# Kernel tuning notes

Hardware: AMD Instinct MI355X
Metric: run time of the kernel (lower is better)

The kernel has to match this reference:

```python
import jax, jax.numpy as jnp
import numpy as np

D_LATENT, D_HIDDEN, D_TIME, K = 128, 256, 16, 3
B, NX = 8, 4096
MSG_IN = 2 * D_LATENT + 1 + D_TIME + 2  # 275
UPD_IN = 2 * D_LATENT + D_TIME          # 272


def _gelu(v):
    return jax.nn.gelu(v, approximate=False)  # torch nn.GELU default (erf)


def _linear_params(key, din, dout):
    k1, k2 = jax.random.split(key)
    bound = 1.0 / np.sqrt(din)
    w = jax.random.uniform(k1, (din, dout), minval=-bound, maxval=bound, dtype=jnp.float32)
    b = jax.random.uniform(k2, (dout,), minval=-bound, maxval=bound, dtype=jnp.float32)
    return w, b


def setup_inputs() -> dict:
    key = jax.random.key(0)
    ks = jax.random.split(key, 16)
    inp = {
        'h': jax.random.normal(ks[0], (B, NX, D_LATENT), dtype=jnp.float32),
        'x': jax.random.uniform(ks[1], (B, NX), dtype=jnp.float32),
        'tau': jax.random.normal(ks[2], (B, D_TIME), dtype=jnp.float32),
        'u0': jax.random.normal(ks[3], (B, NX), dtype=jnp.float32),
    }
    inp['msg_w1'], inp['msg_b1'] = _linear_params(ks[4], MSG_IN, D_HIDDEN)
    inp['msg_w2'], inp['msg_b2'] = _linear_params(ks[5], D_HIDDEN, D_HIDDEN)
    inp['msg_w3'], inp['msg_b3'] = _linear_params(ks[6], D_HIDDEN, D_LATENT)
    inp['gate_w1'], inp['gate_b1'] = _linear_params(ks[7], MSG_IN, D_HIDDEN)
    inp['gate_w2'], inp['gate_b2'] = _linear_params(ks[8], D_HIDDEN, 1)
    inp['upd_w1'], inp['upd_b1'] = _linear_params(ks[9], UPD_IN, D_HIDDEN)
    inp['upd_w2'], inp['upd_b2'] = _linear_params(ks[10], D_HIDDEN, D_HIDDEN)
    inp['upd_w3'], inp['upd_b3'] = _linear_params(ks[11], D_HIDDEN, D_LATENT)
    inp['W_w'], inp['W_b'] = _linear_params(ks[12], D_LATENT, D_LATENT)
    return inp


def reference(h, x, tau, u0, msg_w1, msg_b1, msg_w2, msg_b2, msg_w3, msg_b3,
              gate_w1, gate_b1, gate_w2, gate_b2,
              upd_w1, upd_b1, upd_w2, upd_b2, upd_w3, upd_b3, W_w, W_b):
    Bq, nx, d = h.shape
    k = K
    S = 2 * k + 1
    # replicate padding along the spatial dim
    h_pad = jnp.pad(h, ((0, 0), (k, k), (0, 0)), mode='edge')
    x_pad = jnp.pad(x, ((0, 0), (k, k)), mode='edge')
    u0_pad = jnp.pad(u0, ((0, 0), (k, k)), mode='edge')
    # all stencil windows at once: idx[nx, S] gathers neighbor j for node i
    idx = jnp.arange(nx)[:, None] + jnp.arange(S)[None, :]
    h_j = h_pad[:, idx, :]                                  # [B, nx, S, d]
    rel = (x_pad[:, idx] - x[:, :, None])[..., None]        # [B, nx, S, 1]
    du0 = (u0[:, :, None] - u0_pad[:, idx])[..., None]      # [B, nx, S, 1]
    h_e = jnp.broadcast_to(h[:, :, None, :], (Bq, nx, S, d))
    tau_e = jnp.broadcast_to(tau[:, None, None, :], (Bq, nx, S, tau.shape[-1]))
    msg_in = jnp.concatenate([h_e, h_j, rel, tau_e, du0, jnp.abs(du0)], axis=-1)  # [B,nx,S,275]
    a = _gelu(msg_in @ msg_w1 + msg_b1)
    a = _gelu(a @ msg_w2 + msg_b2)
    msg = a @ msg_w3 + msg_b3                               # [B, nx, S, d]
    g = _gelu(msg_in @ gate_w1 + gate_b1)
    gate = jax.nn.sigmoid(g @ gate_w2 + gate_b2)            # [B, nx, S, 1]
    agg = jnp.sum(gate * msg, axis=2)                       # [B, nx, d]
    tau_n = jnp.broadcast_to(tau[:, None, :], (Bq, nx, tau.shape[-1]))
    upd_in = jnp.concatenate([h, agg, tau_n], axis=-1)      # [B, nx, 272]
    u = _gelu(upd_in @ upd_w1 + upd_b1)
    u = _gelu(u @ upd_w2 + upd_b2)
    h_nonlocal = u @ upd_w3 + upd_b3
    h_local = h @ W_w + W_b
    return _gelu(h_nonlocal + h_local)
```

## Files before the change

kernel.cpp:

```cpp
#include <hip/hip_runtime.h>
#include <hip/hip_bf16.h>
#include <math.h>

#define NXC 4096
#define NNODES 32768

typedef __attribute__((ext_vector_type(8))) short bf16x8;
typedef __attribute__((ext_vector_type(4))) short s16x4;
typedef __attribute__((ext_vector_type(16))) float f32x16;
typedef __attribute__((ext_vector_type(2))) float f32x2;

#define MFMA32(a,b,c) __builtin_amdgcn_mfma_f32_32x32x16_bf16((a),(b),(c),0,0,0)

#define GC4  3.359256e-5f
#define GC3 -0.000850511f
#define GC2  0.00941855f
#define GC1 -0.06622291f
#define GC0  0.3989423f

__device__ __forceinline__ float gelu_f(float x) {
    float xc = fminf(fmaxf(x, -3.0f), 3.0f);
    float s = xc * xc;
    float q = fmaf(s, GC4, GC3);
    q = fmaf(s, q, GC2);
    q = fmaf(s, q, GC1);
    q = fmaf(s, q, GC0);
    return x * fmaf(xc, q, 0.5f);
}
__device__ __forceinline__ f32x2 gelu2(f32x2 x) {
    const f32x2 lo = {-3.0f, -3.0f}, hi = {3.0f, 3.0f};
    const f32x2 c4 = {GC4, GC4}, c3 = {GC3, GC3}, c2 = {GC2, GC2};
    const f32x2 c1 = {GC1, GC1}, c0 = {GC0, GC0}, half = {0.5f, 0.5f};
    f32x2 xc = __builtin_elementwise_min(__builtin_elementwise_max(x, lo), hi);
    f32x2 s = xc * xc;
    f32x2 q = __builtin_elementwise_fma(s, c4, c3);
    q = __builtin_elementwise_fma(s, q, c2);
    q = __builtin_elementwise_fma(s, q, c1);
    q = __builtin_elementwise_fma(s, q, c0);
    return x * __builtin_elementwise_fma(xc, q, half);
}
__device__ __forceinline__ float sigmoid_f(float v) {
    float e = __builtin_amdgcn_exp2f(-1.4426950409f * v);
    return __builtin_amdgcn_rcpf(1.0f + e);
}
__device__ __forceinline__ short f2bs(float x) {
    __hip_bfloat16 b = __float2bfloat16(x);
    union { __hip_bfloat16 h; short s; } u; u.h = b; return u.s;
}
__device__ __forceinline__ f32x16 zero16() {
    f32x16 v;
    #pragma unroll
    for (int i = 0; i < 16; ++i) v[i] = 0.f;
    return v;
}
__device__ __forceinline__ float dpp_xor1(float x) {
    return __int_as_float(__builtin_amdgcn_update_dpp(0, __float_as_int(x), 0xB1, 0xF, 0xF, true));
}
__device__ __forceinline__ float dpp_xor2(float x) {
    return __int_as_float(__builtin_amdgcn_update_dpp(0, __float_as_int(x), 0x4E, 0xF, 0xF, true));
}

__global__ void wconv_kernel(const float* __restrict__ msg_w2, const float* __restrict__ msg_w3,
                             const float* __restrict__ msg_w1, const float* __restrict__ gate_w1,
                             const float* __restrict__ upd_w1, const float* __restrict__ upd_w2,
                             const float* __restrict__ upd_w3, const float* __restrict__ W_w,
                             const float* __restrict__ tau,
                             const float* __restrict__ msg_b1, const float* __restrict__ gate_b1,
                             const float* __restrict__ upd_b1,
                             __hip_bfloat16* __restrict__ w2t, __hip_bfloat16* __restrict__ w3t,
                             __hip_bfloat16* __restrict__ wall_t, __hip_bfloat16* __restrict__ w1ut,
                             __hip_bfloat16* __restrict__ w2ut, __hip_bfloat16* __restrict__ w3ut,
                             __hip_bfloat16* __restrict__ wwt,
                             float* __restrict__ TM, float* __restrict__ TG, float* __restrict__ TU)
{
    if (blockIdx.x >= 1600) {
        const int b = blockIdx.x - 1600;
        const int t = threadIdx.x;
        float tv[16];
        #pragma unroll
        for (int k = 0; k < 16; ++k) tv[k] = tau[b*16 + k];
        float am = msg_b1[t], ag = gate_b1[t], au = upd_b1[t];
        #pragma unroll
        for (int k = 0; k < 16; ++k) {
            am = fmaf(tv[k], msg_w1 [(257+k)*256 + t], am);
            ag = fmaf(tv[k], gate_w1[(257+k)*256 + t], ag);
            au = fmaf(tv[k], upd_w1 [(256+k)*256 + t], au);
        }
        TM[b*256+t] = am; TG[b*256+t] = ag; TU[b*256+t] = au;
        return;
    }
    int i = blockIdx.x * 256 + threadIdx.x;
    if (i < 65536) { int c=i>>8, k=i&255; w2t[i] = __float2bfloat16(msg_w2[k*256+c]); return; }
    i -= 65536;
    if (i < 32768) { int c=i>>8, k=i&255; w3t[i] = __float2bfloat16(msg_w3[k*128+c]); return; }
    i -= 32768;
    if (i < 131072) {
        int c = i>>7, k = i&127; float v;
        if      (c <  256) v = msg_w1 [k*256 + c];
        else if (c <  512) v = msg_w1 [(128+k)*256 + (c-256)];
        else if (c <  768) v = gate_w1[k*256 + (c-512)];
        else               v = gate_w1[(128+k)*256 + (c-768)];
        wall_t[i] = __float2bfloat16(v); return;
    }
    i -= 131072;
    if (i < 65536) { int c=i>>8, k=i&255; w1ut[i] = __float2bfloat16(upd_w1[k*256+c]); return; }
    i -= 65536;
    if (i < 65536) { int c=i>>8, k=i&255; w2ut[i] = __float2bfloat16(upd_w2[k*256+c]); return; }
    i -= 65536;
    if (i < 32768) { int c=i>>8, k=i&255; w3ut[i] = __float2bfloat16(upd_w3[k*128+c]); return; }
    i -= 32768;
    { int c=i>>7, k=i&127; wwt[i] = __float2bfloat16(W_w[k*128+c]); }
}

#define PSTR 136

__global__ __launch_bounds__(256, 3)
void precompute_kernel(const float* __restrict__ h, const __hip_bfloat16* __restrict__ wall_t,
                       __hip_bfloat16* __restrict__ PAm, __hip_bfloat16* __restrict__ PBm,
                       __hip_bfloat16* __restrict__ PAg, __hip_bfloat16* __restrict__ PBg)
{
    __shared__ __align__(16) __hip_bfloat16 hs[64*PSTR];
    __shared__ __align__(16) __hip_bfloat16 ob[64*256];
    const int t = threadIdx.x;
    const int lane = t & 63, wv = t >> 6;
    const int cl = lane & 31, g = lane >> 5;
    const int base = blockIdx.x * 64;

    #pragma unroll
    for (int i = 0; i < 8; ++i) {
        int f = (i*256 + t)*4;
        float4 hv = *(const float4*)&h[(size_t)base*128 + f];
        int row = f >> 7, col = f & 127;
        s16x4 pk; pk[0]=f2bs(hv.x); pk[1]=f2bs(hv.y); pk[2]=f2bs(hv.z); pk[3]=f2bs(hv.w);
        *(s16x4*)&hs[row*PSTR + col] = pk;
    }
    __syncthreads();

    __hip_bfloat16* bufs[4] = {PAm, PBm, PAg, PBg};
    const int c0 = wv*64 + cl, c1 = c0 + 32;
    const __hip_bfloat16* a0  = hs + (size_t)(cl)*PSTR + g*8;
    const __hip_bfloat16* a1p = hs + (size_t)(32+cl)*PSTR + g*8;

    for (int tile = 0; tile < 4; ++tile) {
        f32x16 a00 = zero16(), a01 = zero16(), a10 = zero16(), a11 = zero16();
        {
            const __hip_bfloat16* b0 = wall_t + ((size_t)tile*256 + c0)*128 + g*8;
            const __hip_bfloat16* b1 = wall_t + ((size_t)tile*256 + c1)*128 + g*8;
            #pragma unroll
            for (int kt = 0; kt < 8; ++kt) {
                bf16x8 bf0 = *(const bf16x8*)(b0 + kt*16);
                bf16x8 bf1 = *(const bf16x8*)(b1 + kt*16);
                bf16x8 af0 = *(const bf16x8*)(a0 + kt*16);
                bf16x8 af1 = *(const bf16x8*)(a1p + kt*16);
                a00 = MFMA32(af0, bf0, a00);
                a01 = MFMA32(af0, bf1, a01);
                a10 = MFMA32(af1, bf0, a10);
                a11 = MFMA32(af1, bf1, a11);
            }
        }
        #pragma unroll
        for (int r = 0; r < 16; ++r) {
            int row = (r&3) + 8*(r>>2) + 4*g;
            ob[row*256 + c0]      = __float2bfloat16(a00[r]);
            ob[row*256 + c1]      = __float2bfloat16(a01[r]);
            ob[(32+row)*256 + c0] = __float2bfloat16(a10[r]);
            ob[(32+row)*256 + c1] = __float2bfloat16(a11[r]);
        }
        __syncthreads();
        __hip_bfloat16* dst = bufs[tile];
        #pragma unroll
        for (int i = 0; i < 8; ++i) {
            int idx = i*256 + t;
            int row = idx >> 5, ch = idx & 31;
            *(float4*)&dst[(size_t)(base+row)*256 + ch*8] =
                *(const float4*)&ob[row*256 + ch*8];
        }
        __syncthreads();
    }
}

#define ENPB 8
#define EEPB 56
#define ARS  264
#define MRS  132

__global__ __launch_bounds__(256, 4)
void edge_kernel(const float* __restrict__ x, const float* __restrict__ u0,
                 const float* __restrict__ msg_w1, const float* __restrict__ gate_w1,
                 const __hip_bfloat16* __restrict__ w2t, const float* __restrict__ msg_b2,
                 const __hip_bfloat16* __restrict__ w3t, const float* __restrict__ msg_b3,
                 const float* __restrict__ gate_w2, const float* __restrict__ gate_b2,
                 const __hip_bfloat16* __restrict__ PAm, const __hip_bfloat16* __restrict__ PBm,
                 const __hip_bfloat16* __restrict__ PAg, const __hip_bfloat16* __restrict__ PBg,
                 const float* __restrict__ TM, const float* __restrict__ TG,
                 __hip_bfloat16* __restrict__ AGG)
{
    __shared__ __align__(16) __hip_bfloat16 act[64*ARS];
    __shared__ __align__(16) float s_rel[EEPB], s_du[EEPB], s_ad[EEPB];
    __shared__ float s_gp[4][EEPB];
    __shared__ int   s_slotj[14];
    __shared__ float s_gate[EEPB];

    const int t    = threadIdx.x;
    const int lane = t & 63;
    const int wv   = t >> 6;
    const int base = blockIdx.x * ENPB;
    const int b    = base >> 12;
    const int ii0  = base & (NXC-1);

    if (t < 14) {
        int jj = ii0 - 3 + t;
        jj = jj < 0 ? 0 : (jj > NXC-1 ? NXC-1 : jj);
        s_slotj[t] = b*NXC + jj;
    }
    if (t < EEPB) {
        int nd = t / 7, s = t - nd*7;
        int i  = base + nd;
        int jj = ii0 + nd + s - 3;
        jj = jj < 0 ? 0 : (jj > NXC-1 ? NXC-1 : jj);
        int j = b*NXC + jj;
        float rel = x[j] - x[i];
        float du  = u0[i] - u0[j];
        s_rel[t] = rel; s_du[t] = du; s_ad[t] = fabsf(du);
    }
    __syncthreads();

    {
        float wr  = msg_w1 [256*256+t], wd  = msg_w1 [273*256+t], wa  = msg_w1 [274*256+t];
        float gwr = gate_w1[256*256+t], gwd = gate_w1[273*256+t], gwa = gate_w1[274*256+t];
        float tm = TM[b*256+t], tg = TG[b*256+t];
        float g2 = gate_w2[t];
        const f32x2 wr2  = {wr, wr},  wd2  = {wd, wd},  wa2  = {wa, wa};
        const f32x2 gwr2 = {gwr,gwr}, gwd2 = {gwd,gwd}, gwa2 = {gwa,gwa};
        const f32x2 g22  = {g2, g2};
        float bm[14], bg[14], pam[8], pag[8], sacc[14];
        #pragma unroll
        for (int q = 0; q < 14; ++q) {
            size_t o = (size_t)s_slotj[q]*256 + t;
            bm[q] = __bfloat162float(PBm[o]) + tm;
            bg[q] = __bfloat162float(PBg[o]) + tg;
        }
        #pragma unroll
        for (int nd = 0; nd < 8; ++nd) {
            size_t o = (size_t)(base+nd)*256 + t;
            pam[nd] = __bfloat162float(PAm[o]);
            pag[nd] = __bfloat162float(PAg[o]);
        }
        const bool p1 = (lane & 1), p2 = ((lane & 2) != 0);
        #pragma unroll
        for (int mq = 0; mq < 14; ++mq) {
            float gq[4];
            #pragma unroll
            for (int pp = 0; pp < 2; ++pp) {
                const int e0 = mq*4 + pp*2, e1 = e0 + 1;
                const int nd0 = e0/7, q0 = nd0 + (e0 - nd0*7);
                const int nd1 = e1/7, q1 = nd1 + (e1 - nd1*7);
                f32x2 rel = *(const f32x2*)&s_rel[e0];
                f32x2 du  = *(const f32x2*)&s_du[e0];
                f32x2 ad  = *(const f32x2*)&s_ad[e0];
                f32x2 pm; pm[0] = pam[nd0] + bm[q0]; pm[1] = pam[nd1] + bm[q1];
                pm = __builtin_elementwise_fma(rel, wr2, pm);
                pm = __builtin_elementwise_fma(du,  wd2, pm);
                pm = __builtin_elementwise_fma(ad,  wa2, pm);
                f32x2 gm = gelu2(pm);
                act[e0*ARS + t] = __float2bfloat16(gm[0]);
                act[e1*ARS + t] = __float2bfloat16(gm[1]);
                f32x2 pg; pg[0] = pag[nd0] + bg[q0]; pg[1] = pag[nd1] + bg[q1];
                pg = __builtin_elementwise_fma(rel, gwr2, pg);
                pg = __builtin_elementwise_fma(du,  gwd2, pg);
                pg = __builtin_elementwise_fma(ad,  gwa2, pg);
                f32x2 gg = gelu2(pg) * g22;
                gq[pp*2] = gg[0]; gq[pp*2+1] = gg[1];
            }
            float xx = p1 ? gq[1] : gq[0], yy = p1 ? gq[0] : gq[1];
            xx += dpp_xor1(yy);
            float zz = p1 ? gq[3] : gq[2], ww = p1 ? gq[2] : gq[3];
            zz += dpp_xor1(ww);
            float uu = p2 ? zz : xx, vv = p2 ? xx : zz;
            uu += dpp_xor2(vv);
            sacc[mq] = uu;
        }
        #pragma unroll
        for (int m = 0; m < 14; ++m) {
            float v = sacc[m];
            v += __shfl_xor(v, 4);
            v += __shfl_xor(v, 8);
            v += __shfl_xor(v, 16);
            v += __shfl_xor(v, 32);
            if (lane < 4) s_gp[wv][m*4 + lane] = v;
        }
    }
    __syncthreads();
    if (t < EEPB)
        s_gate[t] = sigmoid_f(s_gp[0][t] + s_gp[1][t] + s_gp[2][t] + s_gp[3][t] + gate_b2[0]);

    const int cl = lane & 31;
    const int g  = lane >> 5;
    f32x16 acc00 = zero16(), acc01 = zero16(), acc10 = zero16(), acc11 = zero16();
    {
        const __hip_bfloat16* w2a = w2t + (size_t)((wv*2+0)*32 + cl)*256 + g*8;
        const __hip_bfloat16* w2b = w2t + (size_t)((wv*2+1)*32 + cl)*256 + g*8;
        const __hip_bfloat16* a1a = act + (size_t)(cl)*ARS + g*8;
        const __hip_bfloat16* a1b = act + (size_t)(32+cl)*ARS + g*8;
        #pragma unroll
        for (int kt = 0; kt < 16; ++kt) {
            bf16x8 bfa = *(const bf16x8*)(w2a + kt*16);
            bf16x8 bfb = *(const bf16x8*)(w2b + kt*16);
            bf16x8 afa = *(const bf16x8*)(a1a + kt*16);
            bf16x8 afb = *(const bf16x8*)(a1b + kt*16);
            acc00 = MFMA32(afa, bfa, acc00);
            acc01 = MFMA32(afa, bfb, acc01);
            acc10 = MFMA32(afb, bfa, acc10);
            acc11 = MFMA32(afb, bfb, acc11);
        }
    }
    __syncthreads();
    {
        const int c0 = (wv*2+0)*32 + cl;
        const int c1 = (wv*2+1)*32 + cl;
        float b20 = msg_b2[c0], b21 = msg_b2[c1];
        #pragma unroll
        for (int r = 0; r < 16; r += 2) {
            int row0 = (r&3) + 8*(r>>2) + 4*g;
            f32x2 v0 = {acc00[r] + b20, acc00[r+1] + b20};
            f32x2 g0 = gelu2(v0);
            act[row0*ARS + c0]     = __float2bfloat16(g0[0]);
            act[(row0+1)*ARS + c0] = __float2bfloat16(g0[1]);
            f32x2 v1 = {acc01[r] + b21, acc01[r+1] + b21};
            f32x2 g1 = gelu2(v1);
            act[row0*ARS + c1]     = __float2bfloat16(g1[0]);
            act[(row0+1)*ARS + c1] = __float2bfloat16(g1[1]);
            if (r < 12) {
                int row1 = 32 + row0;
                f32x2 v2 = {acc10[r] + b20, acc10[r+1] + b20};
                f32x2 g2v = gelu2(v2);
                act[row1*ARS + c0]     = __float2bfloat16(g2v[0]);
                act[(row1+1)*ARS + c0] = __float2bfloat16(g2v[1]);
                f32x2 v3 = {acc11[r] + b21, acc11[r+1] + b21};
                f32x2 g3 = gelu2(v3);
                act[row1*ARS + c1]     = __float2bfloat16(g3[0]);
                act[(row1+1)*ARS + c1] = __float2bfloat16(g3[1]);
            }
        }
    }
    __syncthreads();

    f32x16 m0 = zero16(), m1 = zero16();
    {
        const __hip_bfloat16* w3p = w3t + (size_t)(wv*32 + cl)*256 + g*8;
        const __hip_bfloat16* a2a = act + (size_t)(cl)*ARS + g*8;
        const __hip_bfloat16* a2b = act + (size_t)(32+cl)*ARS + g*8;
        #pragma unroll
        for (int kt = 0; kt < 16; ++kt) {
            bf16x8 bfr = *(const bf16x8*)(w3p + kt*16);
            m0 = MFMA32(*(const bf16x8*)(a2a + kt*16), bfr, m0);
            m1 = MFMA32(*(const bf16x8*)(a2b + kt*16), bfr, m1);
        }
    }
    __syncthreads();
    float* msgbuf = (float*)act;
    {
        const int c = wv*32 + cl;
        float b3v = msg_b3[c];
        #pragma unroll
        for (int r = 0; r < 16; r += 2) {
            int row0 = (r&3) + 8*(r>>2) + 4*g;
            f32x2 mm = {m0[r] + b3v, m0[r+1] + b3v};
            f32x2 gt = {s_gate[row0], s_gate[row0+1]};
            mm *= gt;
            msgbuf[row0*MRS + c]     = mm[0];
            msgbuf[(row0+1)*MRS + c] = mm[1];
            int row1 = 32 + row0;
            if (row1 + 1 < EEPB) {
                f32x2 nn = {m1[r] + b3v, m1[r+1] + b3v};
                f32x2 ht = {s_gate[row1], s_gate[row1+1]};
                nn *= ht;
                msgbuf[row1*MRS + c]     = nn[0];
                msgbuf[(row1+1)*MRS + c] = nn[1];
            }
        }
    }
    __syncthreads();

    {
        const int c2  = (t & 63) * 2;
        const int grp = t >> 6;
        #pragma unroll
        for (int p = 0; p < 2; ++p) {
            int nd = grp + p*4;
            f32x2 s = {0.f, 0.f};
            #pragma unroll
            for (int q2 = 0; q2 < 7; ++q2)
                s += *(const f32x2*)&msgbuf[(nd*7+q2)*MRS + c2];
            ushort2 u;
            u.x = (unsigned short)f2bs(s[0]);
            u.y = (unsigned short)f2bs(s[1]);
            *(ushort2*)&AGG[(size_t)(base+nd)*128 + c2] = u;
        }
    }
}

#define UM 32

__global__ __launch_bounds__(256, 4)
void update_kernel(const __hip_bfloat16* __restrict__ w1ut, const __hip_bfloat16* __restrict__ w2ut,
                   const __hip_bfloat16* __restrict__ w3ut, const __hip_bfloat16* __restrict__ wwt,
                   const float* __restrict__ upd_b2, const float* __restrict__ upd_b3,
                   const float* __restrict__ W_b,
                   const float* __restrict__ h, const __hip_bfloat16* __restrict__ AGG,
                   const float* __restrict__ TU,
                   float* __restrict__ out)
{
    __shared__ __align__(16) __hip_bfloat16 ub[UM*ARS];
    const int t = threadIdx.x;
    const int lane = t & 63, wv = t >> 6;
    const int cl = lane & 31, g = lane >> 5;
    const int base = blockIdx.x * UM;
    const int b = base >> 12;

    #pragma unroll
    for (int i = 0; i < 4; ++i) {
        int f = (i*256 + t)*4;
        int row = f >> 7, col = f & 127;
        float4 hv = *(const float4*)&h[(size_t)base*128 + f];
        s16x4 pk; pk[0]=f2bs(hv.x); pk[1]=f2bs(hv.y); pk[2]=f2bs(hv.z); pk[3]=f2bs(hv.w);
        *(s16x4*)&ub[row*ARS + col] = pk;
    }
    #pragma unroll
    for (int i = 0; i < 2; ++i) {
        int idx = i*256 + t;
        int row = idx >> 4, ch = idx & 15;
        *(float4*)&ub[row*ARS + 128 + ch*8] =
            *(const float4*)&AGG[(size_t)(base+row)*128 + ch*8];
    }
    __syncthreads();

    f32x16 u0a = zero16(), u1a = zero16(), hl = zero16();
    {
        const __hip_bfloat16* a0 = ub + (size_t)(cl)*ARS + g*8;
        const __hip_bfloat16* b0 = w1ut + (size_t)(wv*64 + cl)*256 + g*8;
        const __hip_bfloat16* b1 = w1ut + (size_t)(wv*64 + 32 + cl)*256 + g*8;
        const __hip_bfloat16* bw = wwt + (size_t)(wv*32 + cl)*128 + g*8;
        #pragma unroll
        for (int kt = 0; kt < 16; ++kt) {
            bf16x8 af = *(const bf16x8*)(a0 + kt*16);
            u0a = MFMA32(af, *(const bf16x8*)(b0 + kt*16), u0a);
            u1a = MFMA32(af, *(const bf16x8*)(b1 + kt*16), u1a);
            if (kt < 8)
                hl = MFMA32(af, *(const bf16x8*)(bw + kt*16), hl);
        }
    }
    __syncthreads();
    {
        const int c0 = wv*64 + cl, c1 = c0 + 32;
        float tu0 = TU[b*256 + c0], tu1 = TU[b*256 + c1];
        #pragma unroll
        for (int r = 0; r < 16; r += 2) {
            int row = (r&3) + 8*(r>>2) + 4*g;
            f32x2 v0 = {u0a[r] + tu0, u0a[r+1] + tu0};
            f32x2 g0 = gelu2(v0);
            ub[row*ARS + c0]     = __float2bfloat16(g0[0]);
            ub[(row+1)*ARS + c0] = __float2bfloat16(g0[1]);
            f32x2 v1 = {u1a[r] + tu1, u1a[r+1] + tu1};
            f32x2 g1 = gelu2(v1);
            ub[row*ARS + c1]     = __float2bfloat16(g1[0]);
            ub[(row+1)*ARS + c1] = __float2bfloat16(g1[1]);
        }
    }
    __syncthreads();

    f32x16 v0a = zero16(), v1a = zero16();
    {
        const __hip_bfloat16* a0 = ub + (size_t)(cl)*ARS + g*8;
        const __hip_bfloat16* b0 = w2ut + (size_t)(wv*64 + cl)*256 + g*8;
        const __hip_bfloat16* b1 = w2ut + (size_t)(wv*64 + 32 + cl)*256 + g*8;
        #pragma unroll
        for (int kt = 0; kt < 16; ++kt) {
            bf16x8 af = *(const bf16x8*)(a0 + kt*16);
            v0a = MFMA32(af, *(const bf16x8*)(b0 + kt*16), v0a);
            v1a = MFMA32(af, *(const bf16x8*)(b1 + kt*16), v1a);
        }
    }
    __syncthreads();
    {
        const int c0 = wv*64 + cl, c1 = c0 + 32;
        float b20 = upd_b2[c0], b21 = upd_b2[c1];
        #pragma unroll
        for (int r = 0; r < 16; r += 2) {
            int row = (r&3) + 8*(r>>2) + 4*g;
            f32x2 v0 = {v0a[r] + b20, v0a[r+1] + b20};
            f32x2 g0 = gelu2(v0);
            ub[row*ARS + c0]     = __float2bfloat16(g0[0]);
            ub[(row+1)*ARS + c0] = __float2bfloat16(g0[1]);
            f32x2 v1 = {v1a[r] + b21, v1a[r+1] + b21};
            f32x2 g1 = gelu2(v1);
            ub[row*ARS + c1]     = __float2bfloat16(g1[0]);
            ub[(row+1)*ARS + c1] = __float2bfloat16(g1[1]);
        }
    }
    __syncthreads();

    f32x16 w0a = zero16();
    {
        const __hip_bfloat16* wp = w3ut + (size_t)(wv*32 + cl)*256 + g*8;
        const __hip_bfloat16* a0 = ub + (size_t)(cl)*ARS + g*8;
        #pragma unroll
        for (int kt = 0; kt < 16; ++kt)
            w0a = MFMA32(*(const bf16x8*)(a0 + kt*16), *(const bf16x8*)(wp + kt*16), w0a);
    }
    {
        const int c = wv*32 + cl;
        float b3v = upd_b3[c] + W_b[c];
        #pragma unroll
        for (int r = 0; r < 16; r += 2) {
            int row = (r&3) + 8*(r>>2) + 4*g;
            f32x2 vv = {w0a[r] + b3v + hl[r], w0a[r+1] + b3v + hl[r+1]};
            f32x2 gg = gelu2(vv);
            size_t o0 = (size_t)(base+row)*128 + c;
            size_t o1 = (size_t)(base+row+1)*128 + c;
            out[o0] = gg[0];
            out[o1] = gg[1];
        }
    }
}

extern "C" void kernel_launch(void* const* d_in, const int* in_sizes, int n_in,
                              void* d_out, int out_size, void* d_ws, size_t ws_size,
                              hipStream_t stream)
{
    const float* h      = (const float*)d_in[0];
    const float* x      = (const float*)d_in[1];
    const float* tau    = (const float*)d_in[2];
    const float* u0     = (const float*)d_in[3];
    const float* msg_w1 = (const float*)d_in[4];
    const float* msg_b1 = (const float*)d_in[5];
    const float* msg_w2 = (const float*)d_in[6];
    const float* msg_b2 = (const float*)d_in[7];
    const float* msg_w3 = (const float*)d_in[8];
    const float* msg_b3 = (const float*)d_in[9];
    const float* gate_w1= (const float*)d_in[10];
    const float* gate_b1= (const float*)d_in[11];
    const float* gate_w2= (const float*)d_in[12];
    const float* gate_b2= (const float*)d_in[13];
    const float* upd_w1 = (const float*)d_in[14];
    const float* upd_b1 = (const float*)d_in[15];
    const float* upd_w2 = (const float*)d_in[16];
    const float* upd_b2 = (const float*)d_in[17];
    const float* upd_w3 = (const float*)d_in[18];
    const float* upd_b3 = (const float*)d_in[19];
    const float* W_w    = (const float*)d_in[20];
    const float* W_b    = (const float*)d_in[21];
    float* out = (float*)d_out;

    char* ws = (char*)d_ws;
    size_t off = 0;
    auto alloc = [&](size_t bytes) -> void* {
        void* p = ws + off;
        off += (bytes + 255) & ~(size_t)255;
        return p;
    };
    __hip_bfloat16* PAm = (__hip_bfloat16*)alloc((size_t)NNODES*256*2);
    __hip_bfloat16* PBm = (__hip_bfloat16*)alloc((size_t)NNODES*256*2);
    __hip_bfloat16* PAg = (__hip_bfloat16*)alloc((size_t)NNODES*256*2);
    __hip_bfloat16* PBg = (__hip_bfloat16*)alloc((size_t)NNODES*256*2);
    __hip_bfloat16* AGG = (__hip_bfloat16*)alloc((size_t)NNODES*128*2);
    float* TM  = (float*)alloc(8*256*4);
    float* TG  = (float*)alloc(8*256*4);
    float* TU  = (float*)alloc(8*256*4);
    __hip_bfloat16* w2t   = (__hip_bfloat16*)alloc((size_t)256*256*2);
    __hip_bfloat16* w3t   = (__hip_bfloat16*)alloc((size_t)128*256*2);
    __hip_bfloat16* wall_t= (__hip_bfloat16*)alloc((size_t)1024*128*2);
    __hip_bfloat16* w1ut  = (__hip_bfloat16*)alloc((size_t)256*256*2);
    __hip_bfloat16* w2ut  = (__hip_bfloat16*)alloc((size_t)256*256*2);
    __hip_bfloat16* w3ut  = (__hip_bfloat16*)alloc((size_t)128*256*2);
    __hip_bfloat16* wwt   = (__hip_bfloat16*)alloc((size_t)128*128*2);
    (void)ws_size; (void)in_sizes; (void)n_in; (void)out_size;

    wconv_kernel<<<1608, 256, 0, stream>>>(msg_w2, msg_w3, msg_w1, gate_w1,
                                           upd_w1, upd_w2, upd_w3, W_w,
                                           tau, msg_b1, gate_b1, upd_b1,
                                           w2t, w3t, wall_t, w1ut, w2ut, w3ut, wwt,
                                           TM, TG, TU);
    precompute_kernel<<<NNODES/64, 256, 0, stream>>>(h, wall_t,
                                                     PAm, PBm, PAg, PBg);
    edge_kernel<<<NNODES/ENPB, 256, 0, stream>>>(x, u0, msg_w1, gate_w1,
                                                 w2t, msg_b2, w3t, msg_b3,
                                                 gate_w2, gate_b2,
                                                 PAm, PBm, PAg, PBg, TM, TG, AGG);
    update_kernel<<<NNODES/UM, 256, 0, stream>>>(w1ut, w2ut, w3ut, wwt,
                                                 upd_b2, upd_b3, W_b,
                                                 h, AGG, TU, out);
}
```

Before: 201.3 us.

## Double block size to 512 threads and repartition MFMA tiles across eight waves

Launches the precompute, edge and update kernels with 512 threads instead of 256. Each wave now owns fewer output tiles (one 32-column slice instead of two), so accumulator register pressure drops and more waves share the same LDS tile. The update kernel doubles its rows per block to 64. The edge kernel splits its 56 edges across two thread halves for the layer-1 elementwise work. The intent is better latency hiding and occupancy, at the cost of more per-wave weight-fragment loads and fewer distinct blocks.

```diff
diff --git a/kernel.cpp b/kernel.cpp
--- a/kernel.cpp
+++ b/kernel.cpp
@@ -114,7 +114,7 @@
 
 #define PSTR 136
 
-__global__ __launch_bounds__(256, 3)
+__global__ __launch_bounds__(512, 6)
 void precompute_kernel(const float* __restrict__ h, const __hip_bfloat16* __restrict__ wall_t,
                        __hip_bfloat16* __restrict__ PAm, __hip_bfloat16* __restrict__ PBm,
                        __hip_bfloat16* __restrict__ PAg, __hip_bfloat16* __restrict__ PBg)
@@ -127,8 +127,8 @@
     const int base = blockIdx.x * 64;
 
     #pragma unroll
-    for (int i = 0; i < 8; ++i) {
-        int f = (i*256 + t)*4;
+    for (int i = 0; i < 4; ++i) {
+        int f = (i*512 + t)*4;
         float4 hv = *(const float4*)&h[(size_t)base*128 + f];
         int row = f >> 7, col = f & 127;
         s16x4 pk; pk[0]=f2bs(hv.x); pk[1]=f2bs(hv.y); pk[2]=f2bs(hv.z); pk[3]=f2bs(hv.w);
@@ -137,40 +137,32 @@
     __syncthreads();
 
     __hip_bfloat16* bufs[4] = {PAm, PBm, PAg, PBg};
-    const int c0 = wv*64 + cl, c1 = c0 + 32;
+    const int c0 = wv*32 + cl;
     const __hip_bfloat16* a0  = hs + (size_t)(cl)*PSTR + g*8;
     const __hip_bfloat16* a1p = hs + (size_t)(32+cl)*PSTR + g*8;
 
     for (int tile = 0; tile < 4; ++tile) {
-        f32x16 a00 = zero16(), a01 = zero16(), a10 = zero16(), a11 = zero16();
+        f32x16 acc0 = zero16(), acc1 = zero16();
         {
             const __hip_bfloat16* b0 = wall_t + ((size_t)tile*256 + c0)*128 + g*8;
-            const __hip_bfloat16* b1 = wall_t + ((size_t)tile*256 + c1)*128 + g*8;
             #pragma unroll
             for (int kt = 0; kt < 8; ++kt) {
-                bf16x8 bf0 = *(const bf16x8*)(b0 + kt*16);
-                bf16x8 bf1 = *(const bf16x8*)(b1 + kt*16);
-                bf16x8 af0 = *(const bf16x8*)(a0 + kt*16);
-                bf16x8 af1 = *(const bf16x8*)(a1p + kt*16);
-                a00 = MFMA32(af0, bf0, a00);
-                a01 = MFMA32(af0, bf1, a01);
-                a10 = MFMA32(af1, bf0, a10);
-                a11 = MFMA32(af1, bf1, a11);
+                bf16x8 bf = *(const bf16x8*)(b0 + kt*16);
+                acc0 = MFMA32(*(const bf16x8*)(a0  + kt*16), bf, acc0);
+                acc1 = MFMA32(*(const bf16x8*)(a1p + kt*16), bf, acc1);
             }
         }
         #pragma unroll
         for (int r = 0; r < 16; ++r) {
             int row = (r&3) + 8*(r>>2) + 4*g;
-            ob[row*256 + c0]      = __float2bfloat16(a00[r]);
-            ob[row*256 + c1]      = __float2bfloat16(a01[r]);
-            ob[(32+row)*256 + c0] = __float2bfloat16(a10[r]);
-            ob[(32+row)*256 + c1] = __float2bfloat16(a11[r]);
+            ob[row*256 + c0]      = __float2bfloat16(acc0[r]);
+            ob[(32+row)*256 + c0] = __float2bfloat16(acc1[r]);
         }
         __syncthreads();
         __hip_bfloat16* dst = bufs[tile];
         #pragma unroll
-        for (int i = 0; i < 8; ++i) {
-            int idx = i*256 + t;
+        for (int i = 0; i < 4; ++i) {
+            int idx = i*512 + t;
             int row = idx >> 5, ch = idx & 31;
             *(float4*)&dst[(size_t)(base+row)*256 + ch*8] =
                 *(const float4*)&ob[row*256 + ch*8];
@@ -184,7 +176,7 @@
 #define ARS  264
 #define MRS  132
 
-__global__ __launch_bounds__(256, 4)
+__global__ __launch_bounds__(512, 8)
 void edge_kernel(const float* __restrict__ x, const float* __restrict__ u0,
                  const float* __restrict__ msg_w1, const float* __restrict__ gate_w1,
                  const __hip_bfloat16* __restrict__ w2t, const float* __restrict__ msg_b2,
@@ -197,7 +189,7 @@
 {
     __shared__ __align__(16) __hip_bfloat16 act[64*ARS];
     __shared__ __align__(16) float s_rel[EEPB], s_du[EEPB], s_ad[EEPB];
-    __shared__ float s_gp[4][EEPB];
+    __shared__ float s_gp[8][28];
     __shared__ int   s_slotj[14];
     __shared__ float s_gate[EEPB];
 
@@ -226,46 +218,49 @@
     __syncthreads();
 
     {
-        float wr  = msg_w1 [256*256+t], wd  = msg_w1 [273*256+t], wa  = msg_w1 [274*256+t];
-        float gwr = gate_w1[256*256+t], gwd = gate_w1[273*256+t], gwa = gate_w1[274*256+t];
-        float tm = TM[b*256+t], tg = TG[b*256+t];
-        float g2 = gate_w2[t];
+        const int col  = t & 255;
+        const int half = t >> 8;
+        float wr  = msg_w1 [256*256+col], wd  = msg_w1 [273*256+col], wa  = msg_w1 [274*256+col];
+        float gwr = gate_w1[256*256+col], gwd = gate_w1[273*256+col], gwa = gate_w1[274*256+col];
+        float tm = TM[b*256+col], tg = TG[b*256+col];
+        float g2 = gate_w2[col];
         const f32x2 wr2  = {wr, wr},  wd2  = {wd, wd},  wa2  = {wa, wa};
         const f32x2 gwr2 = {gwr,gwr}, gwd2 = {gwd,gwd}, gwa2 = {gwa,gwa};
         const f32x2 g22  = {g2, g2};
-        float bm[14], bg[14], pam[8], pag[8], sacc[14];
-        #pragma unroll
-        for (int q = 0; q < 14; ++q) {
-            size_t o = (size_t)s_slotj[q]*256 + t;
+        float bm[10], bg[10], pam[4], pag[4], sacc[7];
+        #pragma unroll
+        for (int q = 0; q < 10; ++q) {
+            size_t o = (size_t)s_slotj[half*4 + q]*256 + col;
             bm[q] = __bfloat162float(PBm[o]) + tm;
             bg[q] = __bfloat162float(PBg[o]) + tg;
         }
         #pragma unroll
-        for (int nd = 0; nd < 8; ++nd) {
-            size_t o = (size_t)(base+nd)*256 + t;
-            pam[nd] = __bfloat162float(PAm[o]);
-            pag[nd] = __bfloat162float(PAg[o]);
+        for (int ndl = 0; ndl < 4; ++ndl) {
+            size_t o = (size_t)(base + half*4 + ndl)*256 + col;
+            pam[ndl] = __bfloat162float(PAm[o]);
+            pag[ndl] = __bfloat162float(PAg[o]);
         }
         const bool p1 = (lane & 1), p2 = ((lane & 2) != 0);
         #pragma unroll
-        for (int mq = 0; mq < 14; ++mq) {
+        for (int mq = 0; mq < 7; ++mq) {
             float gq[4];
             #pragma unroll
             for (int pp = 0; pp < 2; ++pp) {
-                const int e0 = mq*4 + pp*2, e1 = e0 + 1;
-                const int nd0 = e0/7, q0 = nd0 + (e0 - nd0*7);
-                const int nd1 = e1/7, q1 = nd1 + (e1 - nd1*7);
+                const int el0 = mq*4 + pp*2, el1 = el0 + 1;
+                const int e0 = half*28 + el0, e1 = e0 + 1;
+                const int ndl0 = el0/7, q0 = ndl0 + (el0 - ndl0*7);
+                const int ndl1 = el1/7, q1 = ndl1 + (el1 - ndl1*7);
                 f32x2 rel = *(const f32x2*)&s_rel[e0];
                 f32x2 du  = *(const f32x2*)&s_du[e0];
                 f32x2 ad  = *(const f32x2*)&s_ad[e0];
-                f32x2 pm; pm[0] = pam[nd0] + bm[q0]; pm[1] = pam[nd1] + bm[q1];
+                f32x2 pm; pm[0] = pam[ndl0] + bm[q0]; pm[1] = pam[ndl1] + bm[q1];
                 pm = __builtin_elementwise_fma(rel, wr2, pm);
                 pm = __builtin_elementwise_fma(du,  wd2, pm);
                 pm = __builtin_elementwise_fma(ad,  wa2, pm);
                 f32x2 gm = gelu2(pm);
-                act[e0*ARS + t] = __float2bfloat16(gm[0]);
-                act[e1*ARS + t] = __float2bfloat16(gm[1]);
-                f32x2 pg; pg[0] = pag[nd0] + bg[q0]; pg[1] = pag[nd1] + bg[q1];
+                act[e0*ARS + col] = __float2bfloat16(gm[0]);
+                act[e1*ARS + col] = __float2bfloat16(gm[1]);
+                f32x2 pg; pg[0] = pag[ndl0] + bg[q0]; pg[1] = pag[ndl1] + bg[q1];
                 pg = __builtin_elementwise_fma(rel, gwr2, pg);
                 pg = __builtin_elementwise_fma(du,  gwd2, pg);
                 pg = __builtin_elementwise_fma(ad,  gwa2, pg);
@@ -281,7 +276,7 @@
             sacc[mq] = uu;
         }
         #pragma unroll
-        for (int m = 0; m < 14; ++m) {
+        for (int m = 0; m < 7; ++m) {
             float v = sacc[m];
             v += __shfl_xor(v, 4);
             v += __shfl_xor(v, 8);
@@ -291,118 +286,94 @@
         }
     }
     __syncthreads();
-    if (t < EEPB)
-        s_gate[t] = sigmoid_f(s_gp[0][t] + s_gp[1][t] + s_gp[2][t] + s_gp[3][t] + gate_b2[0]);
+    if (t < EEPB) {
+        int hf = t / 28, el = t - hf*28;
+        float v = s_gp[hf*4+0][el] + s_gp[hf*4+1][el] + s_gp[hf*4+2][el] + s_gp[hf*4+3][el]
+                + gate_b2[0];
+        s_gate[t] = sigmoid_f(v);
+    }
 
     const int cl = lane & 31;
     const int g  = lane >> 5;
-    f32x16 acc00 = zero16(), acc01 = zero16(), acc10 = zero16(), acc11 = zero16();
-    {
-        const __hip_bfloat16* w2a = w2t + (size_t)((wv*2+0)*32 + cl)*256 + g*8;
-        const __hip_bfloat16* w2b = w2t + (size_t)((wv*2+1)*32 + cl)*256 + g*8;
+    f32x16 acc0 = zero16(), acc1 = zero16();
+    {
+        const __hip_bfloat16* w2p = w2t + (size_t)(wv*32 + cl)*256 + g*8;
         const __hip_bfloat16* a1a = act + (size_t)(cl)*ARS + g*8;
         const __hip_bfloat16* a1b = act + (size_t)(32+cl)*ARS + g*8;
         #pragma unroll
         for (int kt = 0; kt < 16; ++kt) {
-            bf16x8 bfa = *(const bf16x8*)(w2a + kt*16);
-            bf16x8 bfb = *(const bf16x8*)(w2b + kt*16);
-            bf16x8 afa = *(const bf16x8*)(a1a + kt*16);
-            bf16x8 afb = *(const bf16x8*)(a1b + kt*16);
-            acc00 = MFMA32(afa, bfa, acc00);
-            acc01 = MFMA32(afa, bfb, acc01);
-            acc10 = MFMA32(afb, bfa, acc10);
-            acc11 = MFMA32(afb, bfb, acc11);
-        }
-    }
-    __syncthreads();
-    {
-        const int c0 = (wv*2+0)*32 + cl;
-        const int c1 = (wv*2+1)*32 + cl;
-        float b20 = msg_b2[c0], b21 = msg_b2[c1];
+            bf16x8 bf = *(const bf16x8*)(w2p + kt*16);
+            acc0 = MFMA32(*(const bf16x8*)(a1a + kt*16), bf, acc0);
+            acc1 = MFMA32(*(const bf16x8*)(a1b + kt*16), bf, acc1);
+        }
+    }
+    __syncthreads();
+    {
+        const int c0 = wv*32 + cl;
+        float b20 = msg_b2[c0];
         #pragma unroll
         for (int r = 0; r < 16; r += 2) {
             int row0 = (r&3) + 8*(r>>2) + 4*g;
-            f32x2 v0 = {acc00[r] + b20, acc00[r+1] + b20};
+            f32x2 v0 = {acc0[r] + b20, acc0[r+1] + b20};
             f32x2 g0 = gelu2(v0);
             act[row0*ARS + c0]     = __float2bfloat16(g0[0]);
             act[(row0+1)*ARS + c0] = __float2bfloat16(g0[1]);
-            f32x2 v1 = {acc01[r] + b21, acc01[r+1] + b21};
-            f32x2 g1 = gelu2(v1);
-            act[row0*ARS + c1]     = __float2bfloat16(g1[0]);
-            act[(row0+1)*ARS + c1] = __float2bfloat16(g1[1]);
             if (r < 12) {
                 int row1 = 32 + row0;
-                f32x2 v2 = {acc10[r] + b20, acc10[r+1] + b20};
-                f32x2 g2v = gelu2(v2);
-                act[row1*ARS + c0]     = __float2bfloat16(g2v[0]);
-                act[(row1+1)*ARS + c0] = __float2bfloat16(g2v[1]);
-                f32x2 v3 = {acc11[r] + b21, acc11[r+1] + b21};
-                f32x2 g3 = gelu2(v3);
-                act[row1*ARS + c1]     = __float2bfloat16(g3[0]);
-                act[(row1+1)*ARS + c1] = __float2bfloat16(g3[1]);
+                f32x2 v1 = {acc1[r] + b20, acc1[r+1] + b20};
+                f32x2 g1 = gelu2(v1);
+                act[row1*ARS + c0]     = __float2bfloat16(g1[0]);
+                act[(row1+1)*ARS + c0] = __float2bfloat16(g1[1]);
             }
         }
     }
     __syncthreads();
 
-    f32x16 m0 = zero16(), m1 = zero16();
-    {
-        const __hip_bfloat16* w3p = w3t + (size_t)(wv*32 + cl)*256 + g*8;
-        const __hip_bfloat16* a2a = act + (size_t)(cl)*ARS + g*8;
-        const __hip_bfloat16* a2b = act + (size_t)(32+cl)*ARS + g*8;
-        #pragma unroll
-        for (int kt = 0; kt < 16; ++kt) {
-            bf16x8 bfr = *(const bf16x8*)(w3p + kt*16);
-            m0 = MFMA32(*(const bf16x8*)(a2a + kt*16), bfr, m0);
-            m1 = MFMA32(*(const bf16x8*)(a2b + kt*16), bfr, m1);
-        }
+    f32x16 m0 = zero16();
+    const int mt = wv >> 2, nt = wv & 3;
+    {
+        const __hip_bfloat16* w3p = w3t + (size_t)(nt*32 + cl)*256 + g*8;
+        const __hip_bfloat16* a2p = act + (size_t)(mt*32 + cl)*ARS + g*8;
+        #pragma unroll
+        for (int kt = 0; kt < 16; ++kt)
+            m0 = MFMA32(*(const bf16x8*)(a2p + kt*16), *(const bf16x8*)(w3p + kt*16), m0);
     }
     __syncthreads();
     float* msgbuf = (float*)act;
     {
-        const int c = wv*32 + cl;
+        const int c = nt*32 + cl;
         float b3v = msg_b3[c];
         #pragma unroll
         for (int r = 0; r < 16; r += 2) {
-            int row0 = (r&3) + 8*(r>>2) + 4*g;
-            f32x2 mm = {m0[r] + b3v, m0[r+1] + b3v};
-            f32x2 gt = {s_gate[row0], s_gate[row0+1]};
-            mm *= gt;
-            msgbuf[row0*MRS + c]     = mm[0];
-            msgbuf[(row0+1)*MRS + c] = mm[1];
-            int row1 = 32 + row0;
-            if (row1 + 1 < EEPB) {
-                f32x2 nn = {m1[r] + b3v, m1[r+1] + b3v};
-                f32x2 ht = {s_gate[row1], s_gate[row1+1]};
-                nn *= ht;
-                msgbuf[row1*MRS + c]     = nn[0];
-                msgbuf[(row1+1)*MRS + c] = nn[1];
+            int row0 = mt*32 + (r&3) + 8*(r>>2) + 4*g;
+            if (row0 + 1 < EEPB) {
+                f32x2 mm = {m0[r] + b3v, m0[r+1] + b3v};
+                f32x2 gt = {s_gate[row0], s_gate[row0+1]};
+                mm *= gt;
+                msgbuf[row0*MRS + c]     = mm[0];
+                msgbuf[(row0+1)*MRS + c] = mm[1];
             }
         }
     }
     __syncthreads();
 
     {
-        const int c2  = (t & 63) * 2;
-        const int grp = t >> 6;
-        #pragma unroll
-        for (int p = 0; p < 2; ++p) {
-            int nd = grp + p*4;
-            f32x2 s = {0.f, 0.f};
-            #pragma unroll
-            for (int q2 = 0; q2 < 7; ++q2)
-                s += *(const f32x2*)&msgbuf[(nd*7+q2)*MRS + c2];
-            ushort2 u;
-            u.x = (unsigned short)f2bs(s[0]);
-            u.y = (unsigned short)f2bs(s[1]);
-            *(ushort2*)&AGG[(size_t)(base+nd)*128 + c2] = u;
-        }
-    }
-}
-
-#define UM 32
-
-__global__ __launch_bounds__(256, 4)
+        const int c2 = (t & 63) * 2;
+        const int nd = wv;
+        f32x2 s = {0.f, 0.f};
+        #pragma unroll
+        for (int q2 = 0; q2 < 7; ++q2)
+            s += *(const f32x2*)&msgbuf[(nd*7+q2)*MRS + c2];
+        ushort2 u;
+        u.x = (unsigned short)f2bs(s[0]);
+        u.y = (unsigned short)f2bs(s[1]);
+        *(ushort2*)&AGG[(size_t)(base+nd)*128 + c2] = u;
+    }
+}
+
+#define UM 64
+
+__global__ __launch_bounds__(512, 6)
 void update_kernel(const __hip_bfloat16* __restrict__ w1ut, const __hip_bfloat16* __restrict__ w2ut,
                    const __hip_bfloat16* __restrict__ w3ut, const __hip_bfloat16* __restrict__ wwt,
                    const float* __restrict__ upd_b2, const float* __restrict__ upd_b3,
@@ -417,10 +388,11 @@
     const int cl = lane & 31, g = lane >> 5;
     const int base = blockIdx.x * UM;
     const int b = base >> 12;
+    const int mt = wv >> 2, nt = wv & 3;
 
     #pragma unroll
     for (int i = 0; i < 4; ++i) {
-        int f = (i*256 + t)*4;
+        int f = (i*512 + t)*4;
         int row = f >> 7, col = f & 127;
         float4 hv = *(const float4*)&h[(size_t)base*128 + f];
         s16x4 pk; pk[0]=f2bs(hv.x); pk[1]=f2bs(hv.y); pk[2]=f2bs(hv.z); pk[3]=f2bs(hv.w);
@@ -428,7 +400,7 @@
     }
     #pragma unroll
     for (int i = 0; i < 2; ++i) {
-        int idx = i*256 + t;
+        int idx = i*512 + t;
         int row = idx >> 4, ch = idx & 15;
         *(float4*)&ub[row*ARS + 128 + ch*8] =
             *(const float4*)&AGG[(size_t)(base+row)*128 + ch*8];
@@ -437,23 +409,24 @@
 
     f32x16 u0a = zero16(), u1a = zero16(), hl = zero16();
     {
-        const __hip_bfloat16* a0 = ub + (size_t)(cl)*ARS + g*8;
-        const __hip_bfloat16* b0 = w1ut + (size_t)(wv*64 + cl)*256 + g*8;
-        const __hip_bfloat16* b1 = w1ut + (size_t)(wv*64 + 32 + cl)*256 + g*8;
-        const __hip_bfloat16* bw = wwt + (size_t)(wv*32 + cl)*128 + g*8;
+        const __hip_bfloat16* a0  = ub + (size_t)(cl)*ARS + g*8;
+        const __hip_bfloat16* a1p = ub + (size_t)(32+cl)*ARS + g*8;
+        const __hip_bfloat16* ahl = ub + (size_t)(mt*32+cl)*ARS + g*8;
+        const __hip_bfloat16* b0 = w1ut + (size_t)(wv*32 + cl)*256 + g*8;
+        const __hip_bfloat16* bw = wwt + (size_t)(nt*32 + cl)*128 + g*8;
         #pragma unroll
         for (int kt = 0; kt < 16; ++kt) {
-            bf16x8 af = *(const bf16x8*)(a0 + kt*16);
-            u0a = MFMA32(af, *(const bf16x8*)(b0 + kt*16), u0a);
-            u1a = MFMA32(af, *(const bf16x8*)(b1 + kt*16), u1a);
+            bf16x8 bf = *(const bf16x8*)(b0 + kt*16);
+            u0a = MFMA32(*(const bf16x8*)(a0  + kt*16), bf, u0a);
+            u1a = MFMA32(*(const bf16x8*)(a1p + kt*16), bf, u1a);
             if (kt < 8)
-                hl = MFMA32(af, *(const bf16x8*)(bw + kt*16), hl);
-        }
-    }
-    __syncthreads();
-    {
-        const int c0 = wv*64 + cl, c1 = c0 + 32;
-        float tu0 = TU[b*256 + c0], tu1 = TU[b*256 + c1];
+                hl = MFMA32(*(const bf16x8*)(ahl + kt*16), *(const bf16x8*)(bw + kt*16), hl);
+        }
+    }
+    __syncthreads();
+    {
+        const int c0 = wv*32 + cl;
+        float tu0 = TU[b*256 + c0];
         #pragma unroll
         for (int r = 0; r < 16; r += 2) {
             int row = (r&3) + 8*(r>>2) + 4*g;
@@ -461,30 +434,30 @@
             f32x2 g0 = gelu2(v0);
             ub[row*ARS + c0]     = __float2bfloat16(g0[0]);
             ub[(row+1)*ARS + c0] = __float2bfloat16(g0[1]);
-            f32x2 v1 = {u1a[r] + tu1, u1a[r+1] + tu1};
+            f32x2 v1 = {u1a[r] + tu0, u1a[r+1] + tu0};
             f32x2 g1 = gelu2(v1);
-            ub[row*ARS + c1]     = __float2bfloat16(g1[0]);
-            ub[(row+1)*ARS + c1] = __float2bfloat16(g1[1]);
+            ub[(32+row)*ARS + c0]   = __float2bfloat16(g1[0]);
+            ub[(32+row+1)*ARS + c0] = __float2bfloat16(g1[1]);
         }
     }
     __syncthreads();
 
     f32x16 v0a = zero16(), v1a = zero16();
     {
-        const __hip_bfloat16* a0 = ub + (size_t)(cl)*ARS + g*8;
-        const __hip_bfloat16* b0 = w2ut + (size_t)(wv*64 + cl)*256 + g*8;
-        const __hip_bfloat16* b1 = w2ut + (size_t)(wv*64 + 32 + cl)*256 + g*8;
+        const __hip_bfloat16* a0  = ub + (size_t)(cl)*ARS + g*8;
+        const __hip_bfloat16* a1p = ub + (size_t)(32+cl)*ARS + g*8;
+        const __hip_bfloat16* b0 = w2ut + (size_t)(wv*32 + cl)*256 + g*8;
         #pragma unroll
         for (int kt = 0; kt < 16; ++kt) {
-            bf16x8 af = *(const bf16x8*)(a0 + kt*16);
-            v0a = MFMA32(af, *(const bf16x8*)(b0 + kt*16), v0a);
-            v1a = MFMA32(af, *(const bf16x8*)(b1 + kt*16), v1a);
-        }
-    }
-    __syncthreads();
-    {
-        const int c0 = wv*64 + cl, c1 = c0 + 32;
-        float b20 = upd_b2[c0], b21 = upd_b2[c1];
+            bf16x8 bf = *(const bf16x8*)(b0 + kt*16);
+            v0a = MFMA32(*(const bf16x8*)(a0  + kt*16), bf, v0a);
+            v1a = MFMA32(*(const bf16x8*)(a1p + kt*16), bf, v1a);
+        }
+    }
+    __syncthreads();
+    {
+        const int c0 = wv*32 + cl;
+        float b20 = upd_b2[c0];
         #pragma unroll
         for (int r = 0; r < 16; r += 2) {
             int row = (r&3) + 8*(r>>2) + 4*g;
@@ -492,34 +465,32 @@
             f32x2 g0 = gelu2(v0);
             ub[row*ARS + c0]     = __float2bfloat16(g0[0]);
             ub[(row+1)*ARS + c0] = __float2bfloat16(g0[1]);
-            f32x2 v1 = {v1a[r] + b21, v1a[r+1] + b21};
+            f32x2 v1 = {v1a[r] + b20, v1a[r+1] + b20};
             f32x2 g1 = gelu2(v1);
-            ub[row*ARS + c1]     = __float2bfloat16(g1[0]);
-            ub[(row+1)*ARS + c1] = __float2bfloat16(g1[1]);
+            ub[(32+row)*ARS + c0]   = __float2bfloat16(g1[0]);
+            ub[(32+row+1)*ARS + c0] = __float2bfloat16(g1[1]);
         }
     }
     __syncthreads();
 
     f32x16 w0a = zero16();
     {
-        const __hip_bfloat16* wp = w3ut + (size_t)(wv*32 + cl)*256 + g*8;
-        const __hip_bfloat16* a0 = ub + (size_t)(cl)*ARS + g*8;
+        const __hip_bfloat16* wp = w3ut + (size_t)(nt*32 + cl)*256 + g*8;
+        const __hip_bfloat16* a0 = ub + (size_t)(mt*32 + cl)*ARS + g*8;
         #pragma unroll
         for (int kt = 0; kt < 16; ++kt)
             w0a = MFMA32(*(const bf16x8*)(a0 + kt*16), *(const bf16x8*)(wp + kt*16), w0a);
     }
     {
-        const int c = wv*32 + cl;
+        const int c = nt*32 + cl;
         float b3v = upd_b3[c] + W_b[c];
         #pragma unroll
         for (int r = 0; r < 16; r += 2) {
-            int row = (r&3) + 8*(r>>2) + 4*g;
+            int row = mt*32 + (r&3) + 8*(r>>2) + 4*g;
             f32x2 vv = {w0a[r] + b3v + hl[r], w0a[r+1] + b3v + hl[r+1]};
             f32x2 gg = gelu2(vv);
-            size_t o0 = (size_t)(base+row)*128 + c;
-            size_t o1 = (size_t)(base+row+1)*128 + c;
-            out[o0] = gg[0];
-            out[o1] = gg[1];
+            out[(size_t)(base+row)*128 + c]   = gg[0];
+            out[(size_t)(base+row+1)*128 + c] = gg[1];
         }
     }
 }
@@ -581,13 +552,13 @@
                                            tau, msg_b1, gate_b1, upd_b1,
                                            w2t, w3t, wall_t, w1ut, w2ut, w3ut, wwt,
                                            TM, TG, TU);
-    precompute_kernel<<<NNODES/64, 256, 0, stream>>>(h, wall_t,
+    precompute_kernel<<<NNODES/64, 512, 0, stream>>>(h, wall_t,
                                                      PAm, PBm, PAg, PBg);
-    edge_kernel<<<NNODES/ENPB, 256, 0, stream>>>(x, u0, msg_w1, gate_w1,
+    edge_kernel<<<NNODES/ENPB, 512, 0, stream>>>(x, u0, msg_w1, gate_w1,
                                                  w2t, msg_b2, w3t, msg_b3,
                                                  gate_w2, gate_b2,
                                                  PAm, PBm, PAg, PBg, TM, TG, AGG);
-    update_kernel<<<NNODES/UM, 256, 0, stream>>>(w1ut, w2ut, w3ut, wwt,
+    update_kernel<<<NNODES/UM, 512, 0, stream>>>(w1ut, w2ut, w3ut, wwt,
                                                  upd_b2, upd_b3, W_b,
                                                  h, AGG, TU, out);
 }
```

Result: slower. 277.1 us (+37.6%).

## Hoist edge-kernel global loads before barrier and swizzle block order

Applied to the files above, without the earlier changes.

Computes the neighbour slot indices directly in registers, dropping the shared s_slotj table, and issues all PBm/PBg/PAm/PAg and weight loads before the first __syncthreads. These loads can then overlap the rel/du setup and the barrier instead of waiting behind it. It also remaps blockIdx so that consecutive hardware block IDs stride across the grid, likely to spread work across XCDs or L2 slices, and zero-fills the padding rows 56-63 of the act buffer. Holding these values in registers earlier raises register pressure under launch_bounds(256,4). The remap assumes gridDim.x is divisible by 8.

```diff
diff --git a/kernel.cpp b/kernel.cpp
--- a/kernel.cpp
+++ b/kernel.cpp
@@ -198,21 +198,36 @@
     __shared__ __align__(16) __hip_bfloat16 act[64*ARS];
     __shared__ __align__(16) float s_rel[EEPB], s_du[EEPB], s_ad[EEPB];
     __shared__ float s_gp[4][EEPB];
-    __shared__ int   s_slotj[14];
     __shared__ float s_gate[EEPB];
 
     const int t    = threadIdx.x;
     const int lane = t & 63;
     const int wv   = t >> 6;
-    const int base = blockIdx.x * ENPB;
+    const int wg   = ((int)blockIdx.x & 7) * ((int)gridDim.x >> 3) + ((int)blockIdx.x >> 3);
+    const int base = wg * ENPB;
     const int b    = base >> 12;
     const int ii0  = base & (NXC-1);
 
-    if (t < 14) {
-        int jj = ii0 - 3 + t;
+    float bm[14], bg[14], pam[8], pag[8];
+    #pragma unroll
+    for (int q = 0; q < 14; ++q) {
+        int jj = ii0 - 3 + q;
         jj = jj < 0 ? 0 : (jj > NXC-1 ? NXC-1 : jj);
-        s_slotj[t] = b*NXC + jj;
-    }
+        size_t o = ((size_t)(b*NXC + jj))*256 + t;
+        bm[q] = __bfloat162float(PBm[o]);
+        bg[q] = __bfloat162float(PBg[o]);
+    }
+    #pragma unroll
+    for (int nd = 0; nd < 8; ++nd) {
+        size_t o = (size_t)(base+nd)*256 + t;
+        pam[nd] = __bfloat162float(PAm[o]);
+        pag[nd] = __bfloat162float(PAg[o]);
+    }
+    const float wr  = msg_w1 [256*256+t], wd  = msg_w1 [273*256+t], wa  = msg_w1 [274*256+t];
+    const float gwr = gate_w1[256*256+t], gwd = gate_w1[273*256+t], gwa = gate_w1[274*256+t];
+    const float tm = TM[b*256+t], tg = TG[b*256+t];
+    const float g2 = gate_w2[t];
+
     if (t < EEPB) {
         int nd = t / 7, s = t - nd*7;
         int i  = base + nd;
@@ -223,29 +238,18 @@
         float du  = u0[i] - u0[j];
         s_rel[t] = rel; s_du[t] = du; s_ad[t] = fabsf(du);
     }
-    __syncthreads();
-
-    {
-        float wr  = msg_w1 [256*256+t], wd  = msg_w1 [273*256+t], wa  = msg_w1 [274*256+t];
-        float gwr = gate_w1[256*256+t], gwd = gate_w1[273*256+t], gwa = gate_w1[274*256+t];
-        float tm = TM[b*256+t], tg = TG[b*256+t];
-        float g2 = gate_w2[t];
+    {
+        int r = 56 + (t >> 5);
+        float4 z = {0.f, 0.f, 0.f, 0.f};
+        *(float4*)((char*)act + (size_t)r*528 + (size_t)(t & 31)*16) = z;
+    }
+    __syncthreads();
+
+    {
         const f32x2 wr2  = {wr, wr},  wd2  = {wd, wd},  wa2  = {wa, wa};
         const f32x2 gwr2 = {gwr,gwr}, gwd2 = {gwd,gwd}, gwa2 = {gwa,gwa};
         const f32x2 g22  = {g2, g2};
-        float bm[14], bg[14], pam[8], pag[8], sacc[14];
-        #pragma unroll
-        for (int q = 0; q < 14; ++q) {
-            size_t o = (size_t)s_slotj[q]*256 + t;
-            bm[q] = __bfloat162float(PBm[o]) + tm;
-            bg[q] = __bfloat162float(PBg[o]) + tg;
-        }
-        #pragma unroll
-        for (int nd = 0; nd < 8; ++nd) {
-            size_t o = (size_t)(base+nd)*256 + t;
-            pam[nd] = __bfloat162float(PAm[o]);
-            pag[nd] = __bfloat162float(PAg[o]);
-        }
+        float sacc[14];
         const bool p1 = (lane & 1), p2 = ((lane & 2) != 0);
         #pragma unroll
         for (int mq = 0; mq < 14; ++mq) {
@@ -258,14 +262,14 @@
                 f32x2 rel = *(const f32x2*)&s_rel[e0];
                 f32x2 du  = *(const f32x2*)&s_du[e0];
                 f32x2 ad  = *(const f32x2*)&s_ad[e0];
-                f32x2 pm; pm[0] = pam[nd0] + bm[q0]; pm[1] = pam[nd1] + bm[q1];
+                f32x2 pm; pm[0] = pam[nd0] + (bm[q0] + tm); pm[1] = pam[nd1] + (bm[q1] + tm);
                 pm = __builtin_elementwise_fma(rel, wr2, pm);
                 pm = __builtin_elementwise_fma(du,  wd2, pm);
                 pm = __builtin_elementwise_fma(ad,  wa2, pm);
                 f32x2 gm = gelu2(pm);
                 act[e0*ARS + t] = __float2bfloat16(gm[0]);
                 act[e1*ARS + t] = __float2bfloat16(gm[1]);
-                f32x2 pg; pg[0] = pag[nd0] + bg[q0]; pg[1] = pag[nd1] + bg[q1];
+                f32x2 pg; pg[0] = pag[nd0] + (bg[q0] + tg); pg[1] = pag[nd1] + (bg[q1] + tg);
                 pg = __builtin_elementwise_fma(rel, gwr2, pg);
                 pg = __builtin_elementwise_fma(du,  gwd2, pg);
                 pg = __builtin_elementwise_fma(ad,  gwa2, pg);
```

Result: faster. 193.7 us (-3.8%).
